# Kernel optimization log

Measured on AMD Instinct MI355X. Metric: run time of the kernel, lower is better.

Reference implementation:

```python
import jax, jax.numpy as jnp
import numpy as np

MODEL_DIM = 1024
HEAD_SIZE = 128

def setup_inputs() -> dict:
    key = jax.random.key(0)
    k0, k1, k2, k3 = jax.random.split(key, 4)
    embedded = jax.random.normal(k0, (4, 4096, MODEL_DIM), dtype=jnp.float32)
    # nn.Linear(model_dim, head_size, bias=False) weights: [head_size, model_dim]
    s = 1.0 / np.sqrt(MODEL_DIM)
    Wk = jax.random.uniform(k1, (HEAD_SIZE, MODEL_DIM), jnp.float32, -s, s)
    Wq = jax.random.uniform(k2, (HEAD_SIZE, MODEL_DIM), jnp.float32, -s, s)
    Wv = jax.random.uniform(k3, (HEAD_SIZE, MODEL_DIM), jnp.float32, -s, s)
    return {"embedded": embedded, "Wk": Wk, "Wq": Wq, "Wv": Wv}

def reference(embedded, Wk, Wq, Wv):
    # embedded: [b, s, m]; W*: [h, m]
    keys = jnp.einsum('bsm,hm->bsh', embedded, Wk)
    queries = jnp.einsum('bsm,hm->bsh', embedded, Wq)
    values = jnp.einsum('bsm,hm->bsh', embedded, Wv)
    h = keys.shape[-1]
    scores = jnp.einsum('bqh,bkh->bqk', queries, keys) / jnp.sqrt(jnp.float32(h))  # [b,s,s]
    s_len = keys.shape[1]
    causal = jnp.tril(jnp.ones((s_len, s_len), dtype=bool))
    scores = jnp.where(causal, scores, -jnp.inf)
    probs = jax.nn.softmax(scores, axis=-1)
    return jnp.einsum('bqk,bkh->bqh', probs, values)
```

## Files before the change

kernel.cpp:

```cpp
#include <hip/hip_runtime.h>
#include <hip/hip_bf16.h>


#define SEQ 4096
#define BATCH 4
#define HS 128
#define SLOTS_PB 128

typedef unsigned short u16;
typedef __bf16 bf16x8 __attribute__((ext_vector_type(8)));
typedef _Float16 f16x4 __attribute__((ext_vector_type(4)));
typedef float f32x4 __attribute__((ext_vector_type(4)));

__device__ __forceinline__ u16 f2bf(float f) {
    union { float f; unsigned u; } v; v.f = f;
    unsigned u = v.u;
    return (u16)((u + 0x7FFFu + ((u >> 16) & 1u)) >> 16);
}
__device__ __forceinline__ float bf2f(u16 u) {
    union { unsigned u; float f; } v; v.u = ((unsigned)u) << 16; return v.f;
}
__device__ __forceinline__ u16 f2h(float f) {
    union { _Float16 h; u16 u; } v; v.h = (_Float16)f; return v.u;
}
__device__ __forceinline__ void async_cp16(const void* g, void* l) {
    __builtin_amdgcn_global_load_lds(
        (const __attribute__((address_space(1))) unsigned int*)g,
        (__attribute__((address_space(3))) unsigned int*)l, 16, 0, 0);
}
__device__ __forceinline__ int nsplit_of(int Q) {
    return Q / 5 + 1 + (Q >= 23 ? 1 : 0);
}

__global__ __launch_bounds__(256) void wconv_kernel(
    const float* __restrict__ Wk, const float* __restrict__ Wq,
    const float* __restrict__ Wv, u16* __restrict__ Wt)
{
    const int g    = blockIdx.x * 256 + threadIdx.x;
    const int lane = g & 63;
    const int kf   = (g >> 6) & 1;
    const int kc   = (g >> 7) & 15;
    const int nt   = g >> 11;
    const int row  = nt * 16 + (lane & 15);
    const int k0   = kc * 64 + kf * 32 + (lane >> 4) * 8;
    const float* src = (row < 128) ? Wk : ((row < 256) ? Wq : Wv);
    const float scale = (row >= 128 && row < 256)
        ? 0.08838834764831845f * 1.4426950408889634f : 1.0f;
    const float4 v0 = *(const float4*)&src[(size_t)(row & 127) * 1024 + k0];
    const float4 v1 = *(const float4*)&src[(size_t)(row & 127) * 1024 + k0 + 4];
    ushort4 a, b;
    a.x = f2bf(v0.x * scale); a.y = f2bf(v0.y * scale);
    a.z = f2bf(v0.z * scale); a.w = f2bf(v0.w * scale);
    b.x = f2bf(v1.x * scale); b.y = f2bf(v1.y * scale);
    b.z = f2bf(v1.z * scale); b.w = f2bf(v1.w * scale);
    *(ushort4*)&Wt[(size_t)g * 8]     = a;
    *(ushort4*)&Wt[(size_t)g * 8 + 4] = b;
}

__global__ __launch_bounds__(256, 2) void qkv_kernel(
    const float* __restrict__ emb, const u16* __restrict__ Wt,
    u16* __restrict__ Qf, u16* __restrict__ Kf, u16* __restrict__ Vf)
{
    __shared__ u16 sE[2][32][72];
    __shared__ u16 sOut[32][392];

    const int tid  = threadIdx.x;
    const int wv   = tid >> 6;
    const int lane = tid & 63;
    const int quad = lane >> 4;
    const int l16  = lane & 15;
    const int R0   = blockIdx.x * 32;

    const int arow = tid >> 3, ac8 = tid & 7;
    const float* abase = &emb[(size_t)(R0 + arow) * 1024 + ac8 * 8];

    f32x4 acc[2][6];
    #pragma unroll
    for (int rg = 0; rg < 2; rg++)
        #pragma unroll
        for (int nt = 0; nt < 6; nt++) acc[rg][nt] = (f32x4){0.f, 0.f, 0.f, 0.f};

    bf16x8 B0[12], B1[12];

#define LOADB(kci, B)                                                          \
    {                                                                          \
        _Pragma("unroll")                                                      \
        for (int nt = 0; nt < 6; nt++) {                                       \
            const size_t g = ((size_t)((wv * 6 + nt) * 16 + (kci)) * 2) * 64 + lane; \
            B[2 * nt]     = *(const bf16x8*)&Wt[g * 8];                        \
            B[2 * nt + 1] = *(const bf16x8*)&Wt[(g + 64) * 8];                 \
        }                                                                      \
    }
#define WRITEA(buf, v0, v1)                                                    \
    {                                                                          \
        ushort4 lo, hi;                                                        \
        lo.x = f2bf((v0).x); lo.y = f2bf((v0).y);                              \
        lo.z = f2bf((v0).z); lo.w = f2bf((v0).w);                              \
        hi.x = f2bf((v1).x); hi.y = f2bf((v1).y);                              \
        hi.z = f2bf((v1).z); hi.w = f2bf((v1).w);                              \
        *(ushort4*)&sE[buf][arow][ac8 * 8]     = lo;                           \
        *(ushort4*)&sE[buf][arow][ac8 * 8 + 4] = hi;                           \
    }
#define COMPUTE(buf, B)                                                        \
    {                                                                          \
        bf16x8 a[2][2];                                                        \
        _Pragma("unroll")                                                      \
        for (int rg = 0; rg < 2; rg++)                                         \
            _Pragma("unroll")                                                  \
            for (int kf = 0; kf < 2; kf++)                                     \
                a[rg][kf] = *(const bf16x8*)&sE[buf][rg * 16 + l16][kf * 32 + quad * 8]; \
        _Pragma("unroll")                                                      \
        for (int nt = 0; nt < 6; nt++)                                         \
            _Pragma("unroll")                                                  \
            for (int rg = 0; rg < 2; rg++) {                                   \
                acc[rg][nt] = __builtin_amdgcn_mfma_f32_16x16x32_bf16(a[rg][0], B[2 * nt],     acc[rg][nt], 0, 0, 0); \
                acc[rg][nt] = __builtin_amdgcn_mfma_f32_16x16x32_bf16(a[rg][1], B[2 * nt + 1], acc[rg][nt], 0, 0, 0); \
            }                                                                  \
    }

    float4 av0 = *(const float4*)&abase[0];
    float4 av1 = *(const float4*)&abase[4];
    LOADB(0, B0);
    WRITEA(0, av0, av1);

    for (int it = 0; it < 8; it++) {
        const int k1 = 2 * it + 1;
        __syncthreads();
        av0 = *(const float4*)&abase[k1 * 64];
        av1 = *(const float4*)&abase[k1 * 64 + 4];
        LOADB(k1, B1);
        COMPUTE(0, B0);
        WRITEA(1, av0, av1);
        __syncthreads();
        if (it < 7) {
            av0 = *(const float4*)&abase[(k1 + 1) * 64];
            av1 = *(const float4*)&abase[(k1 + 1) * 64 + 4];
            LOADB(k1 + 1, B0);
        }
        COMPUTE(1, B1);
        if (it < 7) WRITEA(0, av0, av1);
    }

    #pragma unroll
    for (int nt = 0; nt < 6; nt++) {
        const int col = wv * 96 + nt * 16 + l16;
        #pragma unroll
        for (int rg = 0; rg < 2; rg++) {
            const int rl = rg * 16 + quad * 4;
            #pragma unroll
            for (int r = 0; r < 4; r++) {
                const float v = acc[rg][nt][r];
                sOut[rl + r][col] = (col < 256) ? f2bf(v) : f2h(v);
            }
        }
    }
    __syncthreads();

    const int b  = R0 >> 12;
    const int s0 = R0 & 4095;
    #pragma unroll
    for (int i = 0; i < 2; i++) {
        const int g    = tid + i * 256;
        const int lg   = g & 63;
        const int kfp  = (g >> 6) & 3;
        const int k16l = g >> 8;
        const int rl   = k16l * 16 + (lg & 15);
        const int cl   = kfp * 32 + (lg >> 4) * 8;
        const size_t base = (((size_t)(b * 256 + (s0 >> 4) + k16l) * 4 + kfp) * 64 + lg) * 8;
        *(uint4*)&Kf[base] = *(const uint4*)&sOut[rl][cl];
        *(uint4*)&Qf[base] = *(const uint4*)&sOut[rl][128 + cl];
    }
    #pragma unroll
    for (int i = 0; i < 4; i++) {
        const int g   = tid + i * 256;
        const int lg  = g & 63;
        const int ntl = (g >> 6) & 1;
        const int ht  = g >> 7;
        const int h   = ht * 16 + (lg & 15);
        const int kl  = ntl * 16 + ((lg >> 4) & 3) * 4;
        ushort4 o;
        o.x = sOut[kl + 0][256 + h];
        o.y = sOut[kl + 1][256 + h];
        o.z = sOut[kl + 2][256 + h];
        o.w = sOut[kl + 3][256 + h];
        const int t64 = s0 >> 6;
        const int ntg = ((s0 >> 4) & 3) + ntl;
        const size_t base = ((((size_t)(b * 64 + t64) * 8 + ht) * 4 + ntg) * 64 + lg) * 4;
        *(ushort4*)&Vf[base] = o;
    }
#undef LOADB
#undef WRITEA
#undef COMPUTE
}

template<bool DIRECT>
__global__ __launch_bounds__(512, 4) void attn_kernel(
    const u16* __restrict__ Qf, const u16* __restrict__ Kf,
    const u16* __restrict__ Vf, u16* __restrict__ Opart,
    float* __restrict__ lpart, float* __restrict__ out)
{
    __shared__ u16 sT[2][16384];

    const int tid  = threadIdx.x;
    const int wv   = tid >> 6;
    const int lane = tid & 63;
    const int quad = lane >> 4;
    const int l16  = lane & 15;

    const int L    = blockIdx.x;
    const int b    = L & 3;
    const int slot = L >> 2;

    int Q = 0, sp = 0;
    if constexpr (DIRECT) {
        Q = slot; sp = 0;
    } else {
        int acc = 0;
        #pragma unroll 1
        for (int qq = 0; qq < 32; ++qq) {
            const int n = nsplit_of(qq);
            if (slot < acc + n) { Q = qq; sp = slot - acc; break; }
            acc += n;
        }
    }
    const int total = 2 * Q + 2;
    const int ns    = DIRECT ? 1 : nsplit_of(Q);
    const int kbeg  = DIRECT ? 0 : (sp * total) / ns;
    const int kend  = DIRECT ? total : ((sp + 1) * total) / ns;

    const int q0 = Q * 128;
    const size_t bS = (size_t)b * SEQ;

    const char* KbB = (const char*)(Kf + (size_t)b * 524288);
    const char* VbB = (const char*)(Vf + (size_t)b * 524288);

    bf16x8 qf[4];
    const int q16 = Q * 8 + wv;
    #pragma unroll
    for (int kf = 0; kf < 4; kf++)
        qf[kf] = *(const bf16x8*)&Qf[(((size_t)(b * 256 + q16) * 4 + kf) * 64 + lane) * 8];

    float rs0 = 0.f;
    f32x4 O[8];
    #pragma unroll
    for (int ht = 0; ht < 8; ht++) O[ht] = (f32x4){0.f, 0.f, 0.f, 0.f};

    const int qg0 = q0 + wv * 16 + l16;

    const int lseg = wv * 1024 + lane * 16;
#define STAGE(bufi, kt)                                                        \
    {                                                                          \
        const char* ks = KbB + (size_t)(kt) * 16384;                           \
        const char* vs = VbB + (size_t)(kt) * 16384;                           \
        char* lb = (char*)&sT[bufi][0] + wv * 1024;                            \
        _Pragma("unroll")                                                      \
        for (int i = 0; i < 2; i++)                                            \
            async_cp16(ks + i * 8192 + lseg, lb + i * 8192);                   \
        _Pragma("unroll")                                                      \
        for (int i = 0; i < 2; i++)                                            \
            async_cp16(vs + i * 8192 + lseg, lb + 16384 + i * 8192);           \
    }

    STAGE(0, kbeg);
    __syncthreads();

    int buf = 0;
    for (int kt = kbeg; kt < kend; ++kt) {
        const int kb = kt * 64;
        if (kt + 1 < kend) STAGE(buf ^ 1, kt + 1);

        const bool diag = (kt >= 2 * Q);
        f16x4 pf0[4];
        #pragma unroll
        for (int nt = 0; nt < 4; nt++) {
            f32x4 s0 = (f32x4){0.f, 0.f, 0.f, 0.f};
            __builtin_amdgcn_s_setprio(1);
            #pragma unroll
            for (int kf = 0; kf < 4; kf++) {
                const bf16x8 kfr = *(const bf16x8*)&sT[buf][((nt * 4 + kf) << 9) + lane * 8];
                s0 = __builtin_amdgcn_mfma_f32_16x16x32_bf16(kfr, qf[kf], s0, 0, 0, 0);
            }
            __builtin_amdgcn_s_setprio(0);
            if (diag) {
                #pragma unroll
                for (int r = 0; r < 4; r++) {
                    const int kg = kb + nt * 16 + quad * 4 + r;
                    if (kg > qg0) s0[r] = -3.0e38f;
                }
            }
            f16x4 p0;
            #pragma unroll
            for (int r = 0; r < 4; r++) {
                const float e0 = exp2f(s0[r] - 4.0f);
                rs0 += e0;
                p0[r] = (_Float16)e0;
            }
            pf0[nt] = p0;
        }

        __builtin_amdgcn_s_setprio(1);
        #pragma unroll
        for (int ht = 0; ht < 8; ht++) {
            f16x4 vf[4];
            #pragma unroll
            for (int nt = 0; nt < 4; nt++)
                vf[nt] = *(const f16x4*)&sT[buf][8192 + ((ht * 4 + nt) << 8) + lane * 4];
            #pragma unroll
            for (int nt = 0; nt < 4; nt++)
                O[ht] = __builtin_amdgcn_mfma_f32_16x16x16f16(vf[nt], pf0[nt], O[ht], 0, 0, 0);
        }
        __builtin_amdgcn_s_setprio(0);

        __syncthreads();
        buf ^= 1;
    }
#undef STAGE

    rs0 += __shfl_xor(rs0, 16); rs0 += __shfl_xor(rs0, 32);

    if constexpr (DIRECT) {
        const float inv = 1.0f / rs0;
        const int q = q0 + wv * 16 + l16;
        #pragma unroll
        for (int ht = 0; ht < 8; ht++) {
            f32x4 o = O[ht] * inv;
            *(f32x4*)&out[(bS + q) * HS + ht * 16 + quad * 4] = o;
        }
    } else {
        const size_t slotbase = (size_t)b * SLOTS_PB + slot;
        #pragma unroll
        for (int ht = 0; ht < 8; ht++) {
            const size_t j = ((slotbase * 8 + wv) * 8 + ht) * 64 + lane;
            ushort4 o;
            o.x = f2bf(O[ht][0]); o.y = f2bf(O[ht][1]);
            o.z = f2bf(O[ht][2]); o.w = f2bf(O[ht][3]);
            *(ushort4*)&Opart[j * 4] = o;
        }
        if (quad == 0)
            lpart[slotbase * 128 + wv * 16 + l16] = rs0;
    }
}

__global__ __launch_bounds__(256) void merge_kernel(
    const u16* __restrict__ Opart, const float* __restrict__ lpart,
    float* __restrict__ out)
{
    const int g    = blockIdx.x * 256 + threadIdx.x;
    const int lane = g & 63;
    const int ht   = (g >> 6) & 7;
    const int wvv  = (g >> 9) & 7;
    const int Q    = (g >> 12) & 31;
    const int b    = g >> 17;
    const int l16  = lane & 15;
    const int qd   = lane >> 4;

    int pre = 0, ns = 0;
    #pragma unroll 1
    for (int qq = 0; qq < 32; ++qq) {
        const int n = nsplit_of(qq);
        if (qq < Q) pre += n;
        else if (qq == Q) { ns = n; break; }
    }
    const size_t base_slot = (size_t)b * SLOTS_PB + pre;
    const int ql = wvv * 16 + l16;

    float den = 0.f;
    f32x4 num = (f32x4){0.f, 0.f, 0.f, 0.f};
    #pragma unroll 1
    for (int s = 0; s < ns; s++) {
        den += lpart[(base_slot + s) * 128 + ql];
        const size_t j = (((base_slot + s) * 8 + wvv) * 8 + ht) * 64 + lane;
        const ushort4 o = *(const ushort4*)&Opart[j * 4];
        num[0] += bf2f(o.x); num[1] += bf2f(o.y);
        num[2] += bf2f(o.z); num[3] += bf2f(o.w);
    }
    const float inv = 1.0f / den;
    float4 o; o.x = num[0] * inv; o.y = num[1] * inv;
    o.z = num[2] * inv; o.w = num[3] * inv;
    const size_t off = ((size_t)b << 19) +
                       (size_t)(Q * 128 + wvv * 16 + l16) * 128 +
                       (size_t)(ht * 4 + qd) * 4;
    *(float4*)&out[off] = o;
}

extern "C" void kernel_launch(void* const* d_in, const int* in_sizes, int n_in,
                              void* d_out, int out_size, void* d_ws, size_t ws_size,
                              hipStream_t stream) {
    const float* emb = (const float*)d_in[0];
    const float* Wk  = (const float*)d_in[1];
    const float* Wq  = (const float*)d_in[2];
    const float* Wv  = (const float*)d_in[3];
    float* out = (float*)d_out;

    char* ws = (char*)d_ws;
    const size_t WBF_SZ    = (size_t)384 * 1024 * 2;
    const size_t QKV_SZ    = (size_t)BATCH * SEQ * HS * 2;
    const size_t Q_OFF     = WBF_SZ;
    const size_t K_OFF     = Q_OFF + QKV_SZ;
    const size_t V_OFF     = K_OFF + QKV_SZ;
    const size_t OPART_OFF = V_OFF + QKV_SZ;
    const size_t OPART_SZ  = (size_t)BATCH * SLOTS_PB * 32768;
    const size_t L_SZ      = (size_t)BATCH * SLOTS_PB * 128 * 4;

    u16* Wt = (u16*)ws;
    u16* Qf = (u16*)(ws + Q_OFF);
    u16* Kf = (u16*)(ws + K_OFF);
    u16* Vf = (u16*)(ws + V_OFF);

    wconv_kernel<<<dim3(192), dim3(256), 0, stream>>>(Wk, Wq, Wv, Wt);
    qkv_kernel<<<dim3(512), dim3(256), 0, stream>>>(emb, Wt, Qf, Kf, Vf);

    const size_t need = OPART_OFF + OPART_SZ + L_SZ;

    if (ws_size >= need) {
        u16*   Opart = (u16*)(ws + OPART_OFF);
        float* lp    = (float*)(ws + OPART_OFF + OPART_SZ);
        attn_kernel<false><<<dim3(4 * SLOTS_PB), dim3(512), 0, stream>>>(Qf, Kf, Vf, Opart, lp, out);
        merge_kernel<<<dim3(BATCH * SEQ * HS / 4 / 256), dim3(256), 0, stream>>>(Opart, lp, out);
    } else {
        attn_kernel<true><<<dim3(32 * BATCH), dim3(512), 0, stream>>>(Qf, Kf, Vf, nullptr, nullptr, out);
    }
}
```

Measured before the change: 160.2 us.

## Use 32-key tiles with triple-buffered async LDS staging

Halves the attention key tile from 64 to 32 keys and moves from double to triple buffering. Loads are issued two tiles ahead and waited on with a partial vmcnt plus a raw barrier instead of a full __syncthreads. This aims to hide global-to-LDS latency better and shrink LDS use per block, at the cost of twice as many loop iterations and barriers. The V address now indexes half-tiles of the existing V layout, and split boundaries are recomputed in the finer units.

```diff
diff --git a/kernel.cpp b/kernel.cpp
--- a/kernel.cpp
+++ b/kernel.cpp
@@ -199,7 +199,7 @@
     const u16* __restrict__ Vf, u16* __restrict__ Opart,
     float* __restrict__ lpart, float* __restrict__ out)
 {
-    __shared__ u16 sT[2][16384];
+    __shared__ u16 sT[3][8192];
 
     const int tid  = threadIdx.x;
     const int wv   = tid >> 6;
@@ -223,7 +223,7 @@
             acc += n;
         }
     }
-    const int total = 2 * Q + 2;
+    const int total = 4 * Q + 4;
     const int ns    = DIRECT ? 1 : nsplit_of(Q);
     const int kbeg  = DIRECT ? 0 : (sp * total) / ns;
     const int kend  = DIRECT ? total : ((sp + 1) * total) / ns;
@@ -247,44 +247,49 @@
 
     const int qg0 = q0 + wv * 16 + l16;
 
-    const int lseg = wv * 1024 + lane * 16;
 #define STAGE(bufi, kt)                                                        \
     {                                                                          \
-        const char* ks = KbB + (size_t)(kt) * 16384;                           \
-        const char* vs = VbB + (size_t)(kt) * 16384;                           \
-        char* lb = (char*)&sT[bufi][0] + wv * 1024;                            \
-        _Pragma("unroll")                                                      \
-        for (int i = 0; i < 2; i++)                                            \
-            async_cp16(ks + i * 8192 + lseg, lb + i * 8192);                   \
-        _Pragma("unroll")                                                      \
-        for (int i = 0; i < 2; i++)                                            \
-            async_cp16(vs + i * 8192 + lseg, lb + 16384 + i * 8192);           \
+        async_cp16(KbB + (size_t)(kt) * 8192 + wv * 1024 + lane * 16,          \
+                   (char*)&sT[bufi][0] + wv * 1024);                           \
+        async_cp16(VbB + ((((size_t)((kt) >> 1) * 8 + wv) * 4 + ((kt) & 1) * 2) << 9) + lane * 16, \
+                   (char*)&sT[bufi][4096] + wv * 1024);                        \
+    }
+#define WAITBAR(N)                                                             \
+    {                                                                          \
+        asm volatile("s_waitcnt vmcnt(" #N ")" ::: "memory");                  \
+        __builtin_amdgcn_sched_barrier(0);                                     \
+        __builtin_amdgcn_s_barrier();                                          \
+        __builtin_amdgcn_sched_barrier(0);                                     \
     }
 
     STAGE(0, kbeg);
-    __syncthreads();
-
-    int buf = 0;
+    STAGE(1, kbeg + 1);
+    WAITBAR(2);
+
+    int bcur = 0;
     for (int kt = kbeg; kt < kend; ++kt) {
-        const int kb = kt * 64;
-        if (kt + 1 < kend) STAGE(buf ^ 1, kt + 1);
-
-        const bool diag = (kt >= 2 * Q);
-        f16x4 pf0[4];
-        #pragma unroll
-        for (int nt = 0; nt < 4; nt++) {
+        const bool more = (kt + 2 < kend);
+        if (more) {
+            const int b2 = (bcur >= 1) ? bcur - 1 : bcur + 2;
+            STAGE(b2, kt + 2);
+        }
+
+        const bool diag = (kt >= 4 * Q);
+        f16x4 pf0[2];
+        #pragma unroll
+        for (int nt = 0; nt < 2; nt++) {
             f32x4 s0 = (f32x4){0.f, 0.f, 0.f, 0.f};
             __builtin_amdgcn_s_setprio(1);
             #pragma unroll
             for (int kf = 0; kf < 4; kf++) {
-                const bf16x8 kfr = *(const bf16x8*)&sT[buf][((nt * 4 + kf) << 9) + lane * 8];
+                const bf16x8 kfr = *(const bf16x8*)&sT[bcur][((nt * 4 + kf) << 9) + lane * 8];
                 s0 = __builtin_amdgcn_mfma_f32_16x16x32_bf16(kfr, qf[kf], s0, 0, 0, 0);
             }
             __builtin_amdgcn_s_setprio(0);
             if (diag) {
                 #pragma unroll
                 for (int r = 0; r < 4; r++) {
-                    const int kg = kb + nt * 16 + quad * 4 + r;
+                    const int kg = kt * 32 + nt * 16 + quad * 4 + r;
                     if (kg > qg0) s0[r] = -3.0e38f;
                 }
             }
@@ -301,20 +306,21 @@
         __builtin_amdgcn_s_setprio(1);
         #pragma unroll
         for (int ht = 0; ht < 8; ht++) {
-            f16x4 vf[4];
+            f16x4 vf[2];
             #pragma unroll
-            for (int nt = 0; nt < 4; nt++)
-                vf[nt] = *(const f16x4*)&sT[buf][8192 + ((ht * 4 + nt) << 8) + lane * 4];
+            for (int nt = 0; nt < 2; nt++)
+                vf[nt] = *(const f16x4*)&sT[bcur][4096 + ((ht * 2 + nt) << 8) + lane * 4];
             #pragma unroll
-            for (int nt = 0; nt < 4; nt++)
+            for (int nt = 0; nt < 2; nt++)
                 O[ht] = __builtin_amdgcn_mfma_f32_16x16x16f16(vf[nt], pf0[nt], O[ht], 0, 0, 0);
         }
         __builtin_amdgcn_s_setprio(0);
 
-        __syncthreads();
-        buf ^= 1;
+        if (more) { WAITBAR(2); } else { WAITBAR(0); }
+        bcur = (bcur == 2) ? 0 : bcur + 1;
     }
 #undef STAGE
+#undef WAITBAR
 
     rs0 += __shfl_xor(rs0, 16); rs0 += __shfl_xor(rs0, 32);
 
```

Result: no change. 159.5 us, median of 2 (-0.4%).
